# Kernel tuning notes

Measured on AMD Instinct MI355X. Metric: run time of the kernel, lower is better.

## Reference

```python
import jax, jax.numpy as jnp
import numpy as np

EPS = 1e-5

def _bn(h, g, b):
    # BatchNorm1d with batch statistics (biased variance), eps=1e-5
    m = jnp.mean(h, axis=0)
    v = jnp.var(h, axis=0)
    return (h - m) * jax.lax.rsqrt(v + EPS) * g + b

def setup_inputs() -> dict:
    key = jax.random.key(0)
    ks = jax.random.split(key, 12)
    N, E, F = 100000, 500000, 128
    D = 2 * F  # 256
    s = 1.0 / np.sqrt(D)
    inp = {
        "x": jax.random.normal(ks[0], (N, F), dtype=jnp.float32),
        "edge_index": jax.random.randint(ks[1], (2, E), 0, N, dtype=jnp.int64),
        "W4": jax.random.normal(ks[2], (D, D), jnp.float32) * s,
        "b4": jnp.zeros((D,), jnp.float32),
        "g4": jnp.ones((D,), jnp.float32),
        "be4": jnp.zeros((D,), jnp.float32),
        "W1": jax.random.normal(ks[3], (D, D), jnp.float32) * s,
        "b1": jnp.zeros((D,), jnp.float32),
        "g1": jnp.ones((D,), jnp.float32),
        "be1": jnp.zeros((D,), jnp.float32),
        "W2": jax.random.normal(ks[4], (D, D), jnp.float32) * s,
        "b2": jnp.zeros((D,), jnp.float32),
        "g2": jnp.ones((D,), jnp.float32),
        "be2": jnp.zeros((D,), jnp.float32),
        "Wf": jax.random.normal(ks[5], (D, 1), jnp.float32) * s,
        "bf": jnp.zeros((1,), jnp.float32),
    }
    return inp

def reference(x, edge_index, W4, b4, g4, be4, W1, b1, g1, be1, W2, b2, g2, be2, Wf, bf):
    # gather + concat: [E, 2*F]
    edge_x = jnp.concatenate((x[edge_index[0]], x[edge_index[1]]), axis=1)
    # block 4: Linear -> BN -> ReLU (dropout = identity in eval)
    edge_x = jax.nn.relu(_bn(edge_x @ W4 + b4, g4, be4))
    # block 1 with residual
    out1 = jax.nn.relu(_bn(edge_x @ W1 + b1, g1, be1)) + edge_x
    # block 2 with residual
    out2 = jax.nn.relu(_bn(out1 @ W2 + b2, g2, be2)) + out1
    # final projection -> flatten to [E]
    return jnp.ravel(out2 @ Wf + bf)
```

## Files before the change

kernel.cpp:

```cpp
#include <hip/hip_runtime.h>
#include <hip/hip_bf16.h>
#include <stdint.h>


typedef __attribute__((ext_vector_type(8))) short short8;
typedef __attribute__((ext_vector_type(4))) float f32x4;

__device__ __forceinline__ unsigned short bf16b(float f) {
  unsigned int u = __float_as_uint(f);
  return (unsigned short)((u + 0x7fffu + ((u >> 16) & 1u)) >> 16);
}
__device__ __forceinline__ unsigned int packbf(float lo, float hi) {
  return (unsigned int)bf16b(lo) | ((unsigned int)bf16b(hi) << 16);
}
__device__ __forceinline__ float bflo(unsigned int u) { return __uint_as_float(u << 16); }
__device__ __forceinline__ float bfhi(unsigned int u) { return __uint_as_float(u & 0xffff0000u); }
__device__ __forceinline__ float bfs(short s) { return __uint_as_float(((unsigned int)(unsigned short)s) << 16); }
__device__ __forceinline__ float relu_(float x) { return fmaxf(x, 0.0f); }

__global__ __launch_bounds__(256) void k_init(const int* __restrict__ ei,
                                              float* __restrict__ stats, int* __restrict__ flag) {
  const int t = threadIdx.x;
  for (int i = t; i < 1536; i += 256) stats[i] = 0.f;
  if (t == 0) {
    int o = 0;
#pragma unroll
    for (int i = 0; i < 32; ++i) o |= ei[2 * i + 1];
    *flag = (o == 0) ? 1 : 0;
  }
}

__global__ __launch_bounds__(256) void k_seed(float* __restrict__ out, const float* __restrict__ bfp, int E) {
  const int i = blockIdx.x * 256 + threadIdx.x;
  if (i < E) out[i] = bfp[0];
}

__global__ __launch_bounds__(256) void k_prep(
    const float* __restrict__ W4, const float* __restrict__ W1, const float* __restrict__ W2,
    unsigned short* __restrict__ wt4, unsigned short* __restrict__ wt1, unsigned short* __restrict__ wt2)
{
  const int b = blockIdx.x;
  const int t = threadIdx.x;
  const int wi = b >> 6;
  const int r = b & 63;
  const float* W = (wi == 0) ? W4 : (wi == 1) ? W1 : W2;
  unsigned short* Wt = (wi == 0) ? wt4 : (wi == 1) ? wt1 : wt2;
  const int flat = r * 1024 + t * 4;
  const int n = flat >> 8;
  const int k = flat & 255;
  ushort4 o;
  o.x = bf16b(W[(k + 0) * 256 + n]);
  o.y = bf16b(W[(k + 1) * 256 + n]);
  o.z = bf16b(W[(k + 2) * 256 + n]);
  o.w = bf16b(W[(k + 3) * 256 + n]);
  *(ushort4*)(Wt + flat) = o;
}

__global__ __launch_bounds__(256) void k_stats(
    const float* __restrict__ stats, const float* __restrict__ g, const float* __restrict__ be,
    const float* __restrict__ bias, float* __restrict__ scale, float invE)
{
  const int c = threadIdx.x;
  const float mean = stats[c] * invE;
  const float var = stats[256 + c] * invE - mean * mean;
  const float a = g[c] * rsqrtf(var + 1e-5f);
  const float cstd = be[c] - mean * a;
  scale[c] = a;
  scale[256 + c] = cstd;
  scale[512 + c] = fmaf(a, bias[c], cstd);
}

template<int MODE>
__global__ __launch_bounds__(512, 1) void kp(
    const void* Asrc, const int* __restrict__ ei, const int* __restrict__ flagp,
    const unsigned short* __restrict__ Wt, const float* __restrict__ bias,
    const float* __restrict__ scst, const float* __restrict__ scep, const float* __restrict__ wf,
    unsigned short* __restrict__ buf, float* __restrict__ stats, float* __restrict__ out,
    int E, int MT)
{
  __shared__ __align__(16) char bB[131072];
  __shared__ __align__(16) char aT[32768];

  const int t = threadIdx.x;
  const int b = blockIdx.x;
  const int per = MT >> 8, rem = MT & 255;
  const int t0 = b * per + (b < rem ? b : rem);
  const int t1 = t0 + per + (b < rem ? 1 : 0);

  const int l = t & 63, wv = t >> 6;
  const int wr = wv >> 2, wc = wv & 3;
  const int sw = (l & 7) << 4;
  const int subc = t & 31, rB = t >> 5;
  const int colb = wc * 64 + (l & 15);
  const int lr0 = wr * 32 + ((l >> 4) << 2);
  const int flag = (MODE == 1) ? flagp[0] : 0;

  float bj[4];
  if (MODE != 3) {
#pragma unroll
    for (int j = 0; j < 4; ++j) bj[j] = bias[colb + j * 16];
  }
  float aS[8], cS[8];
  if (MODE == 2) {
#pragma unroll
    for (int k = 0; k < 8; ++k) { aS[k] = scst[subc * 8 + k]; cS[k] = scst[512 + subc * 8 + k]; }
  }
  float aE[4], cE[4], wE[4];
  if (MODE == 3) {
#pragma unroll
    for (int j = 0; j < 4; ++j) {
      const int c = colb + j * 16;
      aE[j] = scep[c]; cE[j] = scep[512 + c]; wE[j] = wf[c];
    }
  }
  float ssum[4] = {0.f, 0.f, 0.f, 0.f}, ssq[4] = {0.f, 0.f, 0.f, 0.f};

  uint4 pf[4];
#define PREFETCH(TT)                                                              \
  if (MODE == 1) {                                                                \
    const float* xf = (const float*)Asrc;                                         \
    _Pragma("unroll")                                                             \
    for (int r = 0; r < 4; ++r) {                                                 \
      const int row = rB + r * 16;                                                \
      int e = (TT) * 64 + row; if (e >= E) e = E - 1;                             \
      const int idx = (subc < 16) ? e : (E + e);                                  \
      const int node = flag ? ei[2 * idx] : ei[idx];                              \
      const float* s = xf + node * 128 + (subc & 15) * 8;                         \
      float4 f0 = *(const float4*)s;                                              \
      float4 f1 = *(const float4*)(s + 4);                                        \
      pf[r].x = packbf(f0.x, f0.y); pf[r].y = packbf(f0.z, f0.w);                 \
      pf[r].z = packbf(f1.x, f1.y); pf[r].w = packbf(f1.z, f1.w);                 \
    }                                                                             \
  } else {                                                                        \
    const uint4* s = (const uint4*)((const char*)Asrc + (size_t)(TT) * 32768);    \
    _Pragma("unroll")                                                             \
    for (int r = 0; r < 4; ++r) pf[r] = s[t + r * 512];                           \
  }

#define STAGE_A                                                                   \
  _Pragma("unroll")                                                               \
  for (int r = 0; r < 4; ++r) {                                                   \
    const int row = rB + r * 16;                                                  \
    uint4 v = pf[r];                                                              \
    if (MODE == 2) {                                                              \
      unsigned int* vp = (unsigned int*)&v;                                       \
      _Pragma("unroll")                                                           \
      for (int h2 = 0; h2 < 4; ++h2) {                                            \
        float lo = relu_(fmaf(bflo(vp[h2]), aS[h2 * 2], cS[h2 * 2]));             \
        float hi = relu_(fmaf(bfhi(vp[h2]), aS[h2 * 2 + 1], cS[h2 * 2 + 1]));     \
        vp[h2] = packbf(lo, hi);                                                  \
      }                                                                           \
    }                                                                             \
    *(uint4*)(aT + row * 512 + ((subc * 16) ^ ((row & 7) << 4))) = v;             \
  }

  PREFETCH(t0);
#pragma unroll
  for (int r = 0; r < 16; ++r) {
    const int c = t + r * 512;
    uint4 v = *(const uint4*)(Wt + c * 8);
    const int n = c >> 5;
    *(uint4*)(bB + n * 512 + (((c & 31) * 16) ^ ((n & 7) << 4))) = v;
  }
  STAGE_A;
  __syncthreads();

  const int ar = wr * 32 + (l & 15);
  const int bn = wc * 64 + (l & 15);

  for (int tt = t0;;) {
    const bool more = (tt + 1 < t1);
    if (more) PREFETCH(tt + 1);

    f32x4 acc[2][4];
    f32x4 zz = {0.f, 0.f, 0.f, 0.f};
#pragma unroll
    for (int i = 0; i < 2; ++i)
#pragma unroll
      for (int j = 0; j < 4; ++j) acc[i][j] = zz;

#pragma unroll
    for (int ks = 0; ks < 4; ++ks) {
#pragma unroll
      for (int kk = 0; kk < 2; ++kk) {
        const int kb = ks * 128 + kk * 64 + ((l >> 4) << 4);
        short8 af[2], bfr[4];
        af[0] = *(const short8*)(aT + ar * 512 + (kb ^ sw));
        af[1] = *(const short8*)(aT + (ar + 16) * 512 + (kb ^ sw));
#pragma unroll
        for (int j = 0; j < 4; ++j)
          bfr[j] = *(const short8*)(bB + (bn + j * 16) * 512 + (kb ^ sw));
#pragma unroll
        for (int i = 0; i < 2; ++i)
#pragma unroll
          for (int j = 0; j < 4; ++j)
            acc[i][j] = __builtin_amdgcn_mfma_f32_16x16x32_bf16(af[i], bfr[j], acc[i][j], 0, 0, 0);
      }
    }

    if (MODE != 3) {
#pragma unroll
      for (int i = 0; i < 2; ++i) {
        const int r0 = tt * 64 + lr0 + i * 16;
#pragma unroll
        for (int j = 0; j < 4; ++j) {
#pragma unroll
          for (int q = 0; q < 4; ++q) {
            const float v = acc[i][j][q] + bj[j];
            if (r0 + q < E) { ssum[j] += v; ssq[j] = fmaf(v, v, ssq[j]); }
          }
        }
      }
    } else {
      float dq[2][4];
#pragma unroll
      for (int i = 0; i < 2; ++i)
#pragma unroll
        for (int q = 0; q < 4; ++q) dq[i][q] = 0.f;
#pragma unroll
      for (int i = 0; i < 2; ++i) {
#pragma unroll
        for (int j = 0; j < 4; ++j) {
#pragma unroll
          for (int q = 0; q < 4; ++q) {
            const int lrow = lr0 + i * 16 + q;
            const float h = bfs(*(const short*)(aT + lrow * 512 +
                                (((colb + j * 16) * 2) ^ ((lrow & 7) << 4))));
            const float v = relu_(fmaf(acc[i][j][q], aE[j], cE[j])) + h;
            acc[i][j][q] = v;
            dq[i][q] = fmaf(v, wE[j], dq[i][q]);
          }
        }
      }
#pragma unroll
      for (int i = 0; i < 2; ++i)
#pragma unroll
        for (int q = 0; q < 4; ++q) {
          float p = dq[i][q];
          p += __shfl_xor(p, 1); p += __shfl_xor(p, 2); p += __shfl_xor(p, 4); p += __shfl_xor(p, 8);
          if ((l & 15) == 0) {
            const int row = tt * 64 + lr0 + i * 16 + q;
            if (row < E) atomicAdd(&out[row], p);
          }
        }
    }
    __syncthreads();

    if (MODE != 2) {
      const int odd = l & 1;
#pragma unroll
      for (int i = 0; i < 2; ++i) {
        const int r0 = lr0 + i * 16;
#pragma unroll
        for (int j = 0; j < 4; ++j) {
          float v0 = acc[i][j][0], v1 = acc[i][j][1], v2 = acc[i][j][2], v3 = acc[i][j][3];
          float p0 = __shfl_xor(v0, 1), p1 = __shfl_xor(v1, 1);
          float p2 = __shfl_xor(v2, 1), p3 = __shfl_xor(v3, 1);
          float loA = odd ? p2 : v0, hiA = odd ? v2 : p0;
          float loB = odd ? p3 : v1, hiB = odd ? v3 : p1;
          const int ra = r0 + (odd ? 2 : 0);
          const int cp2 = ((colb + j * 16) & ~1) * 2;
          *(unsigned int*)(aT + (ra + 0) * 512 + (cp2 ^ (((ra + 0) & 7) << 4))) = packbf(loA, hiA);
          *(unsigned int*)(aT + (ra + 1) * 512 + (cp2 ^ (((ra + 1) & 7) << 4))) = packbf(loB, hiB);
        }
      }
      __syncthreads();
    }

    {
      char* d = (char*)buf + (size_t)tt * 32768;
#pragma unroll
      for (int r = 0; r < 4; ++r) {
        const int c = t + r * 512;
        const int row = c >> 5;
        uint4 v = *(const uint4*)(aT + row * 512 + (((c & 31) * 16) ^ ((row & 7) << 4)));
        *(uint4*)(d + c * 16) = v;
      }
    }

    ++tt;
    if (!(tt < t1)) break;
    __syncthreads();
    STAGE_A;
    __syncthreads();
  }

  if (MODE != 3) {
#pragma unroll
    for (int j = 0; j < 4; ++j) {
      ssum[j] += __shfl_xor(ssum[j], 16); ssum[j] += __shfl_xor(ssum[j], 32);
      ssq[j]  += __shfl_xor(ssq[j], 16);  ssq[j]  += __shfl_xor(ssq[j], 32);
    }
    const int g = l >> 4;
    float sg = (g == 0) ? ssum[0] : (g == 1) ? ssum[1] : (g == 2) ? ssum[2] : ssum[3];
    float qg = (g == 0) ? ssq[0] : (g == 1) ? ssq[1] : (g == 2) ? ssq[2] : ssq[3];
    const int col = wc * 64 + g * 16 + (l & 15);
    atomicAdd(&stats[col], sg);
    atomicAdd(&stats[256 + col], qg);
  }
#undef PREFETCH
#undef STAGE_A
}

__global__ __launch_bounds__(512) void k_fin(
    const unsigned short* __restrict__ Y, const float* __restrict__ scale,
    const float* __restrict__ wf, float* __restrict__ out, int E)
{
  __shared__ float sS[768];
  const int t = threadIdx.x;
  if (t < 256) { sS[t] = scale[t]; sS[256 + t] = scale[512 + t]; sS[512 + t] = wf[t]; }
  __syncthreads();
  const int row = blockIdx.x * 64 + (t >> 3);
  const int p = t & 7;
  const unsigned short* r = Y + (size_t)row * 256 + p * 32;
  float acc = 0.f;
#pragma unroll
  for (int m = 0; m < 4; ++m) {
    uint4 v = *(const uint4*)(r + m * 8);
    const int k0 = p * 32 + m * 8;
    const unsigned int* vp = (const unsigned int*)&v;
#pragma unroll
    for (int h = 0; h < 4; ++h) {
      const int k = k0 + h * 2;
      acc = fmaf(relu_(fmaf(bflo(vp[h]), sS[k], sS[256 + k])), sS[512 + k], acc);
      acc = fmaf(relu_(fmaf(bfhi(vp[h]), sS[k + 1], sS[256 + k + 1])), sS[512 + k + 1], acc);
    }
  }
  acc += __shfl_xor(acc, 1); acc += __shfl_xor(acc, 2); acc += __shfl_xor(acc, 4);
  if (p == 0 && row < E) out[row] += acc;
}

__global__ __launch_bounds__(256) void k_bail(float* __restrict__ out, const float* __restrict__ bfp, int E) {
  const int i = blockIdx.x * 256 + threadIdx.x;
  if (i < E) out[i] = bfp[0];
}

extern "C" void kernel_launch(void* const* d_in, const int* in_sizes, int n_in,
                              void* d_out, int out_size, void* d_ws, size_t ws_size,
                              hipStream_t stream) {
  const float* x   = (const float*)d_in[0];
  const int*   ei  = (const int*)d_in[1];
  const float* W4  = (const float*)d_in[2];
  const float* b4  = (const float*)d_in[3];
  const float* g4  = (const float*)d_in[4];
  const float* be4 = (const float*)d_in[5];
  const float* W1  = (const float*)d_in[6];
  const float* b1  = (const float*)d_in[7];
  const float* g1  = (const float*)d_in[8];
  const float* be1 = (const float*)d_in[9];
  const float* W2  = (const float*)d_in[10];
  const float* b2  = (const float*)d_in[11];
  const float* g2  = (const float*)d_in[12];
  const float* be2 = (const float*)d_in[13];
  const float* Wf  = (const float*)d_in[14];
  const float* bfp = (const float*)d_in[15];
  float* out = (float*)d_out;

  const int E = out_size;
  const int MT = (E + 63) / 64;
  const float invE = 1.0f / (float)E;

  char* ws = (char*)d_ws;
  unsigned short* wt4 = (unsigned short*)(ws);
  unsigned short* wt1 = (unsigned short*)(ws + 131072);
  unsigned short* wt2 = (unsigned short*)(ws + 262144);
  float* stats = (float*)(ws + 393216);
  float* scale = (float*)(ws + 399360);
  int*   flag  = (int*)(ws + 408576);
  const size_t fixed = 409600;
  const size_t bufbytes = (size_t)MT * 32768;
  unsigned short* buf = (unsigned short*)(ws + fixed);

  if (ws_size < fixed + bufbytes) {
    k_bail<<<(E + 255) / 256, 256, 0, stream>>>(out, bfp, E);
    return;
  }

  k_init<<<1, 256, 0, stream>>>(ei, stats, flag);
  k_prep<<<192, 256, 0, stream>>>(W4, W1, W2, wt4, wt1, wt2);

  kp<1><<<256, 512, 0, stream>>>((const void*)x, ei, flag, wt4, b4,
                                 nullptr, nullptr, nullptr, buf, stats, nullptr, E, MT);
  k_stats<<<1, 256, 0, stream>>>(stats, g4, be4, b4, scale, invE);
  kp<2><<<256, 512, 0, stream>>>((const void*)buf, nullptr, flag, wt1, b1,
                                 scale, nullptr, nullptr, buf, stats + 512, nullptr, E, MT);
  k_stats<<<1, 256, 0, stream>>>(stats + 512, g1, be1, b1, scale + 768, invE);
  k_seed<<<(E + 255) / 256, 256, 0, stream>>>(out, bfp, E);
  kp<3><<<256, 512, 0, stream>>>((const void*)buf, nullptr, flag, wt1, nullptr,
                                 nullptr, scale + 768, Wf, buf, nullptr, out, E, MT);
  kp<4><<<256, 512, 0, stream>>>((const void*)buf, nullptr, flag, wt2, b2,
                                 nullptr, nullptr, nullptr, buf, stats + 1024, nullptr, E, MT);
  k_stats<<<1, 256, 0, stream>>>(stats + 1024, g2, be2, b2, scale + 1536, invE);
  k_fin<<<MT, 512, 0, stream>>>(buf, scale + 1536, Wf, out, E);
}
```

Measured before the change: 610.2 us.

## Double-buffer A tiles, hold B fragments in registers, use 1024-thread blocks

The GEMM kernel now runs 1024 threads per block with 16 waves. Each wave keeps its slice of the weight matrix in registers, loaded once, so the B operand is no longer re-read from LDS on every tile. The A tile is double-buffered in LDS so staging the next tile overlaps the MFMA work on the current one. Mode 3 now applies the BN transform itself, and its final-projection partial sums are reduced in LDS and written directly, replacing the global atomics and the separate seed kernel. BN statistics go into 8 slices of atomics to cut contention. The cost is higher register pressure, and the LDS reduction needs extra barriers per tile.

Result: slower. 1.011 ms (+65.7%).

```diff
diff --git a/kernel.cpp b/kernel.cpp
--- a/kernel.cpp
+++ b/kernel.cpp
@@ -21,7 +21,7 @@
 __global__ __launch_bounds__(256) void k_init(const int* __restrict__ ei,
                                               float* __restrict__ stats, int* __restrict__ flag) {
   const int t = threadIdx.x;
-  for (int i = t; i < 1536; i += 256) stats[i] = 0.f;
+  for (int i = t; i < 12288; i += 256) stats[i] = 0.f;
   if (t == 0) {
     int o = 0;
 #pragma unroll
@@ -30,7 +30,7 @@
   }
 }
 
-__global__ __launch_bounds__(256) void k_seed(float* __restrict__ out, const float* __restrict__ bfp, int E) {
+__global__ __launch_bounds__(256) void k_bail(float* __restrict__ out, const float* __restrict__ bfp, int E) {
   const int i = blockIdx.x * 256 + threadIdx.x;
   if (i < E) out[i] = bfp[0];
 }
@@ -61,8 +61,11 @@
     const float* __restrict__ bias, float* __restrict__ scale, float invE)
 {
   const int c = threadIdx.x;
-  const float mean = stats[c] * invE;
-  const float var = stats[256 + c] * invE - mean * mean;
+  float s = 0.f, q = 0.f;
+#pragma unroll
+  for (int sl = 0; sl < 8; ++sl) { s += stats[sl * 512 + c]; q += stats[sl * 512 + 256 + c]; }
+  const float mean = s * invE;
+  const float var = q * invE - mean * mean;
   const float a = g[c] * rsqrtf(var + 1e-5f);
   const float cstd = be[c] - mean * a;
   scale[c] = a;
@@ -71,15 +74,15 @@
 }
 
 template<int MODE>
-__global__ __launch_bounds__(512, 1) void kp(
+__global__ __launch_bounds__(1024, 1) void kp(
     const void* Asrc, const int* __restrict__ ei, const int* __restrict__ flagp,
     const unsigned short* __restrict__ Wt, const float* __restrict__ bias,
     const float* __restrict__ scst, const float* __restrict__ scep, const float* __restrict__ wf,
     unsigned short* __restrict__ buf, float* __restrict__ stats, float* __restrict__ out,
-    int E, int MT)
+    const float* __restrict__ bfp, int E, int MT)
 {
-  __shared__ __align__(16) char bB[131072];
-  __shared__ __align__(16) char aT[32768];
+  __shared__ __align__(16) char lds[131072];
+  float* sRed = (float*)(lds + 65536);
 
   const int t = threadIdx.x;
   const int b = blockIdx.x;
@@ -88,114 +91,119 @@
   const int t1 = t0 + per + (b < rem ? 1 : 0);
 
   const int l = t & 63, wv = t >> 6;
-  const int wr = wv >> 2, wc = wv & 3;
+  const int wr = wv >> 3, wc = wv & 7;
   const int sw = (l & 7) << 4;
-  const int subc = t & 31, rB = t >> 5;
-  const int colb = wc * 64 + (l & 15);
+  const int subc = t & 31;
+  const int colb = wc * 32 + (l & 15);
   const int lr0 = wr * 32 + ((l >> 4) << 2);
   const int flag = (MODE == 1) ? flagp[0] : 0;
-
-  float bj[4];
-  if (MODE != 3) {
-#pragma unroll
-    for (int j = 0; j < 4; ++j) bj[j] = bias[colb + j * 16];
-  }
-  float aS[8], cS[8];
-  if (MODE == 2) {
-#pragma unroll
-    for (int k = 0; k < 8; ++k) { aS[k] = scst[subc * 8 + k]; cS[k] = scst[512 + subc * 8 + k]; }
-  }
-  float aE[4], cE[4], wE[4];
+  const float bf0 = (MODE == 3) ? bfp[0] : 0.f;
+
+  float bj[2];
+  if (MODE != 3) { bj[0] = bias[colb]; bj[1] = bias[colb + 16]; }
+  float aE[2], cE[2], wE[2];
   if (MODE == 3) {
 #pragma unroll
-    for (int j = 0; j < 4; ++j) {
+    for (int j = 0; j < 2; ++j) {
       const int c = colb + j * 16;
       aE[j] = scep[c]; cE[j] = scep[512 + c]; wE[j] = wf[c];
     }
   }
-  float ssum[4] = {0.f, 0.f, 0.f, 0.f}, ssq[4] = {0.f, 0.f, 0.f, 0.f};
-
-  uint4 pf[4];
-#define PREFETCH(TT)                                                              \
-  if (MODE == 1) {                                                                \
-    const float* xf = (const float*)Asrc;                                         \
-    _Pragma("unroll")                                                             \
-    for (int r = 0; r < 4; ++r) {                                                 \
-      const int row = rB + r * 16;                                                \
-      int e = (TT) * 64 + row; if (e >= E) e = E - 1;                             \
-      const int idx = (subc < 16) ? e : (E + e);                                  \
-      const int node = flag ? ei[2 * idx] : ei[idx];                              \
-      const float* s = xf + node * 128 + (subc & 15) * 8;                         \
-      float4 f0 = *(const float4*)s;                                              \
-      float4 f1 = *(const float4*)(s + 4);                                        \
-      pf[r].x = packbf(f0.x, f0.y); pf[r].y = packbf(f0.z, f0.w);                 \
-      pf[r].z = packbf(f1.x, f1.y); pf[r].w = packbf(f1.z, f1.w);                 \
-    }                                                                             \
-  } else {                                                                        \
-    const uint4* s = (const uint4*)((const char*)Asrc + (size_t)(TT) * 32768);    \
-    _Pragma("unroll")                                                             \
-    for (int r = 0; r < 4; ++r) pf[r] = s[t + r * 512];                           \
-  }
-
-#define STAGE_A                                                                   \
-  _Pragma("unroll")                                                               \
-  for (int r = 0; r < 4; ++r) {                                                   \
-    const int row = rB + r * 16;                                                  \
-    uint4 v = pf[r];                                                              \
-    if (MODE == 2) {                                                              \
-      unsigned int* vp = (unsigned int*)&v;                                       \
-      _Pragma("unroll")                                                           \
-      for (int h2 = 0; h2 < 4; ++h2) {                                            \
-        float lo = relu_(fmaf(bflo(vp[h2]), aS[h2 * 2], cS[h2 * 2]));             \
-        float hi = relu_(fmaf(bfhi(vp[h2]), aS[h2 * 2 + 1], cS[h2 * 2 + 1]));     \
-        vp[h2] = packbf(lo, hi);                                                  \
-      }                                                                           \
-    }                                                                             \
-    *(uint4*)(aT + row * 512 + ((subc * 16) ^ ((row & 7) << 4))) = v;             \
+  float ssum[2] = {0.f, 0.f}, ssq[2] = {0.f, 0.f};
+
+  uint4 pf[2];
+#define PREFETCH(TT)                                                            \
+  if (MODE == 1) {                                                              \
+    const float* xf = (const float*)Asrc;                                       \
+    _Pragma("unroll")                                                           \
+    for (int r = 0; r < 2; ++r) {                                               \
+      const int c = t + r * 1024;                                               \
+      const int row = c >> 5;                                                   \
+      int e = (TT) * 64 + row; if (e >= E) e = E - 1;                           \
+      const int idx = (subc < 16) ? e : (E + e);                                \
+      const int node = flag ? ei[2 * idx] : ei[idx];                            \
+      const float* s = xf + node * 128 + (subc & 15) * 8;                       \
+      float4 f0 = *(const float4*)s;                                            \
+      float4 f1 = *(const float4*)(s + 4);                                      \
+      pf[r].x = packbf(f0.x, f0.y); pf[r].y = packbf(f0.z, f0.w);               \
+      pf[r].z = packbf(f1.x, f1.y); pf[r].w = packbf(f1.z, f1.w);               \
+    }                                                                           \
+  } else {                                                                      \
+    const uint4* s = (const uint4*)((const char*)Asrc + (size_t)(TT) * 32768);  \
+    pf[0] = s[t]; pf[1] = s[t + 1024];                                          \
+  }
+
+#define STAGE_A(AP)                                                             \
+  _Pragma("unroll")                                                             \
+  for (int r = 0; r < 2; ++r) {                                                 \
+    const int c = t + r * 1024;                                                 \
+    const int row = c >> 5;                                                     \
+    uint4 v = pf[r];                                                            \
+    if (MODE == 2 || MODE == 3) {                                               \
+      const float4* s4 = (const float4*)(scst + subc * 8);                      \
+      const float4* c4 = (const float4*)(scst + 512 + subc * 8);                \
+      float4 aa0 = s4[0], aa1 = s4[1], cc0 = c4[0], cc1 = c4[1];                \
+      unsigned int* vp = (unsigned int*)&v;                                     \
+      vp[0] = packbf(relu_(fmaf(bflo(vp[0]), aa0.x, cc0.x)),                    \
+                     relu_(fmaf(bfhi(vp[0]), aa0.y, cc0.y)));                   \
+      vp[1] = packbf(relu_(fmaf(bflo(vp[1]), aa0.z, cc0.z)),                    \
+                     relu_(fmaf(bfhi(vp[1]), aa0.w, cc0.w)));                   \
+      vp[2] = packbf(relu_(fmaf(bflo(vp[2]), aa1.x, cc1.x)),                    \
+                     relu_(fmaf(bfhi(vp[2]), aa1.y, cc1.y)));                   \
+      vp[3] = packbf(relu_(fmaf(bflo(vp[3]), aa1.z, cc1.z)),                    \
+                     relu_(fmaf(bfhi(vp[3]), aa1.w, cc1.w)));                   \
+    }                                                                           \
+    *(uint4*)((AP) + row * 512 + ((subc * 16) ^ ((row & 7) << 4))) = v;         \
   }
 
   PREFETCH(t0);
 #pragma unroll
-  for (int r = 0; r < 16; ++r) {
-    const int c = t + r * 512;
+  for (int r = 0; r < 8; ++r) {
+    const int c = t + r * 1024;
     uint4 v = *(const uint4*)(Wt + c * 8);
     const int n = c >> 5;
-    *(uint4*)(bB + n * 512 + (((c & 31) * 16) ^ ((n & 7) << 4))) = v;
-  }
-  STAGE_A;
+    *(uint4*)(lds + n * 512 + (((c & 31) * 16) ^ ((n & 7) << 4))) = v;
+  }
   __syncthreads();
-
-  const int ar = wr * 32 + (l & 15);
-  const int bn = wc * 64 + (l & 15);
-
-  for (int tt = t0;;) {
-    const bool more = (tt + 1 < t1);
-    if (more) PREFETCH(tt + 1);
-
-    f32x4 acc[2][4];
+  short8 bf8[8][2];
+#pragma unroll
+  for (int s8 = 0; s8 < 8; ++s8) {
+    const int kb = (s8 * 64 + ((l >> 4) << 4)) ^ sw;
+#pragma unroll
+    for (int j = 0; j < 2; ++j) {
+      const int bn = wc * 32 + j * 16 + (l & 15);
+      bf8[s8][j] = *(const short8*)(lds + bn * 512 + kb);
+    }
+  }
+  __syncthreads();
+  char* aT0 = lds;
+  char* aT1 = lds + 32768;
+
+  STAGE_A(aT0);
+  if (t0 + 1 < t1) PREFETCH(t0 + 1);
+  __syncthreads();
+
+  int cur = 0;
+  for (int tt = t0; tt < t1; ++tt) {
+    char* aC = cur ? aT1 : aT0;
+    char* aN = cur ? aT0 : aT1;
+    if (tt + 1 < t1) {
+      STAGE_A(aN);
+      if (tt + 2 < t1) PREFETCH(tt + 2);
+    }
+
+    f32x4 acc[2][2];
     f32x4 zz = {0.f, 0.f, 0.f, 0.f};
-#pragma unroll
-    for (int i = 0; i < 2; ++i)
-#pragma unroll
-      for (int j = 0; j < 4; ++j) acc[i][j] = zz;
-
-#pragma unroll
-    for (int ks = 0; ks < 4; ++ks) {
-#pragma unroll
-      for (int kk = 0; kk < 2; ++kk) {
-        const int kb = ks * 128 + kk * 64 + ((l >> 4) << 4);
-        short8 af[2], bfr[4];
-        af[0] = *(const short8*)(aT + ar * 512 + (kb ^ sw));
-        af[1] = *(const short8*)(aT + (ar + 16) * 512 + (kb ^ sw));
-#pragma unroll
-        for (int j = 0; j < 4; ++j)
-          bfr[j] = *(const short8*)(bB + (bn + j * 16) * 512 + (kb ^ sw));
-#pragma unroll
-        for (int i = 0; i < 2; ++i)
-#pragma unroll
-          for (int j = 0; j < 4; ++j)
-            acc[i][j] = __builtin_amdgcn_mfma_f32_16x16x32_bf16(af[i], bfr[j], acc[i][j], 0, 0, 0);
-      }
+    acc[0][0] = zz; acc[0][1] = zz; acc[1][0] = zz; acc[1][1] = zz;
+#pragma unroll
+    for (int s8 = 0; s8 < 8; ++s8) {
+      const int kb = (s8 * 64 + ((l >> 4) << 4)) ^ sw;
+      short8 a0 = *(const short8*)(aC + (wr * 32 + (l & 15)) * 512 + kb);
+      short8 a1 = *(const short8*)(aC + (wr * 32 + 16 + (l & 15)) * 512 + kb);
+      acc[0][0] = __builtin_amdgcn_mfma_f32_16x16x32_bf16(a0, bf8[s8][0], acc[0][0], 0, 0, 0);
+      acc[0][1] = __builtin_amdgcn_mfma_f32_16x16x32_bf16(a0, bf8[s8][1], acc[0][1], 0, 0, 0);
+      acc[1][0] = __builtin_amdgcn_mfma_f32_16x16x32_bf16(a1, bf8[s8][0], acc[1][0], 0, 0, 0);
+      acc[1][1] = __builtin_amdgcn_mfma_f32_16x16x32_bf16(a1, bf8[s8][1], acc[1][1], 0, 0, 0);
     }
 
     if (MODE != 3) {
@@ -203,13 +211,12 @@
       for (int i = 0; i < 2; ++i) {
         const int r0 = tt * 64 + lr0 + i * 16;
 #pragma unroll
-        for (int j = 0; j < 4; ++j) {
+        for (int j = 0; j < 2; ++j)
 #pragma unroll
           for (int q = 0; q < 4; ++q) {
             const float v = acc[i][j][q] + bj[j];
             if (r0 + q < E) { ssum[j] += v; ssq[j] = fmaf(v, v, ssq[j]); }
           }
-        }
       }
     } else {
       float dq[2][4];
@@ -218,30 +225,27 @@
 #pragma unroll
         for (int q = 0; q < 4; ++q) dq[i][q] = 0.f;
 #pragma unroll
-      for (int i = 0; i < 2; ++i) {
-#pragma unroll
-        for (int j = 0; j < 4; ++j) {
+      for (int i = 0; i < 2; ++i)
+#pragma unroll
+        for (int j = 0; j < 2; ++j) {
+          const int col = colb + j * 16;
 #pragma unroll
           for (int q = 0; q < 4; ++q) {
             const int lrow = lr0 + i * 16 + q;
-            const float h = bfs(*(const short*)(aT + lrow * 512 +
-                                (((colb + j * 16) * 2) ^ ((lrow & 7) << 4))));
+            const float h = bfs(*(const short*)(aC + lrow * 512 + ((col * 2) ^ ((lrow & 7) << 4))));
             const float v = relu_(fmaf(acc[i][j][q], aE[j], cE[j])) + h;
             acc[i][j][q] = v;
             dq[i][q] = fmaf(v, wE[j], dq[i][q]);
           }
         }
-      }
 #pragma unroll
       for (int i = 0; i < 2; ++i)
 #pragma unroll
         for (int q = 0; q < 4; ++q) {
           float p = dq[i][q];
-          p += __shfl_xor(p, 1); p += __shfl_xor(p, 2); p += __shfl_xor(p, 4); p += __shfl_xor(p, 8);
-          if ((l & 15) == 0) {
-            const int row = tt * 64 + lr0 + i * 16 + q;
-            if (row < E) atomicAdd(&out[row], p);
-          }
+          p += __shfl_xor(p, 1); p += __shfl_xor(p, 2);
+          p += __shfl_xor(p, 4); p += __shfl_xor(p, 8);
+          if ((l & 15) == 0) sRed[(lr0 + i * 16 + q) * 8 + wc] = p;
         }
     }
     __syncthreads();
@@ -252,7 +256,7 @@
       for (int i = 0; i < 2; ++i) {
         const int r0 = lr0 + i * 16;
 #pragma unroll
-        for (int j = 0; j < 4; ++j) {
+        for (int j = 0; j < 2; ++j) {
           float v0 = acc[i][j][0], v1 = acc[i][j][1], v2 = acc[i][j][2], v3 = acc[i][j][3];
           float p0 = __shfl_xor(v0, 1), p1 = __shfl_xor(v1, 1);
           float p2 = __shfl_xor(v2, 1), p3 = __shfl_xor(v3, 1);
@@ -260,43 +264,49 @@
           float loB = odd ? p3 : v1, hiB = odd ? v3 : p1;
           const int ra = r0 + (odd ? 2 : 0);
           const int cp2 = ((colb + j * 16) & ~1) * 2;
-          *(unsigned int*)(aT + (ra + 0) * 512 + (cp2 ^ (((ra + 0) & 7) << 4))) = packbf(loA, hiA);
-          *(unsigned int*)(aT + (ra + 1) * 512 + (cp2 ^ (((ra + 1) & 7) << 4))) = packbf(loB, hiB);
+          *(unsigned int*)(aC + (ra + 0) * 512 + (cp2 ^ (((ra + 0) & 7) << 4))) = packbf(loA, hiA);
+          *(unsigned int*)(aC + (ra + 1) * 512 + (cp2 ^ (((ra + 1) & 7) << 4))) = packbf(loB, hiB);
+        }
+      }
+      if (MODE == 3 && t < 64) {
+        const int row = tt * 64 + t;
+        if (row < E) {
+          float s = 0.f;
+#pragma unroll
+          for (int w = 0; w < 8; ++w) s += sRed[t * 8 + w];
+          out[row] = s + bf0;
         }
       }
       __syncthreads();
-    }
-
-    {
       char* d = (char*)buf + (size_t)tt * 32768;
 #pragma unroll
-      for (int r = 0; r < 4; ++r) {
-        const int c = t + r * 512;
+      for (int r = 0; r < 2; ++r) {
+        const int c = t + r * 1024;
         const int row = c >> 5;
-        uint4 v = *(const uint4*)(aT + row * 512 + (((c & 31) * 16) ^ ((row & 7) << 4)));
+        uint4 v = *(const uint4*)(aC + row * 512 + (((c & 31) * 16) ^ ((row & 7) << 4)));
         *(uint4*)(d + c * 16) = v;
       }
-    }
-
-    ++tt;
-    if (!(tt < t1)) break;
-    __syncthreads();
-    STAGE_A;
-    __syncthreads();
+      __syncthreads();
+    }
+    cur ^= 1;
   }
 
   if (MODE != 3) {
 #pragma unroll
-    for (int j = 0; j < 4; ++j) {
+    for (int j = 0; j < 2; ++j) {
       ssum[j] += __shfl_xor(ssum[j], 16); ssum[j] += __shfl_xor(ssum[j], 32);
       ssq[j]  += __shfl_xor(ssq[j], 16);  ssq[j]  += __shfl_xor(ssq[j], 32);
     }
     const int g = l >> 4;
-    float sg = (g == 0) ? ssum[0] : (g == 1) ? ssum[1] : (g == 2) ? ssum[2] : ssum[3];
-    float qg = (g == 0) ? ssq[0] : (g == 1) ? ssq[1] : (g == 2) ? ssq[2] : ssq[3];
-    const int col = wc * 64 + g * 16 + (l & 15);
-    atomicAdd(&stats[col], sg);
-    atomicAdd(&stats[256 + col], qg);
+    const int col = wc * 32 + ((g & 1) << 4) + (l & 15);
+    const float val = (g < 2) ? ((g & 1) ? ssum[1] : ssum[0]) : ((g & 1) ? ssq[1] : ssq[0]);
+    __syncthreads();
+    sRed[wr * 512 + ((g >> 1) << 8) + col] = val;
+    __syncthreads();
+    if (t < 512) {
+      const float v = sRed[t] + sRed[512 + t];
+      atomicAdd(&stats[(b & 7) * 512 + t], v);
+    }
   }
 #undef PREFETCH
 #undef STAGE_A
@@ -328,11 +338,6 @@
   }
   acc += __shfl_xor(acc, 1); acc += __shfl_xor(acc, 2); acc += __shfl_xor(acc, 4);
   if (p == 0 && row < E) out[row] += acc;
-}
-
-__global__ __launch_bounds__(256) void k_bail(float* __restrict__ out, const float* __restrict__ bfp, int E) {
-  const int i = blockIdx.x * 256 + threadIdx.x;
-  if (i < E) out[i] = bfp[0];
 }
 
 extern "C" void kernel_launch(void* const* d_in, const int* in_sizes, int n_in,
@@ -365,9 +370,9 @@
   unsigned short* wt1 = (unsigned short*)(ws + 131072);
   unsigned short* wt2 = (unsigned short*)(ws + 262144);
   float* stats = (float*)(ws + 393216);
-  float* scale = (float*)(ws + 399360);
-  int*   flag  = (int*)(ws + 408576);
-  const size_t fixed = 409600;
+  float* scale = (float*)(ws + 442368);
+  int*   flag  = (int*)(ws + 451584);
+  const size_t fixed = 458752;
   const size_t bufbytes = (size_t)MT * 32768;
   unsigned short* buf = (unsigned short*)(ws + fixed);
 
@@ -379,17 +384,16 @@
   k_init<<<1, 256, 0, stream>>>(ei, stats, flag);
   k_prep<<<192, 256, 0, stream>>>(W4, W1, W2, wt4, wt1, wt2);
 
-  kp<1><<<256, 512, 0, stream>>>((const void*)x, ei, flag, wt4, b4,
-                                 nullptr, nullptr, nullptr, buf, stats, nullptr, E, MT);
+  kp<1><<<256, 1024, 0, stream>>>((const void*)x, ei, flag, wt4, b4,
+                                  nullptr, nullptr, nullptr, buf, stats, nullptr, bfp, E, MT);
   k_stats<<<1, 256, 0, stream>>>(stats, g4, be4, b4, scale, invE);
-  kp<2><<<256, 512, 0, stream>>>((const void*)buf, nullptr, flag, wt1, b1,
-                                 scale, nullptr, nullptr, buf, stats + 512, nullptr, E, MT);
-  k_stats<<<1, 256, 0, stream>>>(stats + 512, g1, be1, b1, scale + 768, invE);
-  k_seed<<<(E + 255) / 256, 256, 0, stream>>>(out, bfp, E);
-  kp<3><<<256, 512, 0, stream>>>((const void*)buf, nullptr, flag, wt1, nullptr,
-                                 nullptr, scale + 768, Wf, buf, nullptr, out, E, MT);
-  kp<4><<<256, 512, 0, stream>>>((const void*)buf, nullptr, flag, wt2, b2,
-                                 nullptr, nullptr, nullptr, buf, stats + 1024, nullptr, E, MT);
-  k_stats<<<1, 256, 0, stream>>>(stats + 1024, g2, be2, b2, scale + 1536, invE);
+  kp<2><<<256, 1024, 0, stream>>>((const void*)buf, nullptr, flag, wt1, b1,
+                                  scale, nullptr, nullptr, buf, stats + 4096, nullptr, bfp, E, MT);
+  k_stats<<<1, 256, 0, stream>>>(stats + 4096, g1, be1, b1, scale + 768, invE);
+  kp<3><<<256, 1024, 0, stream>>>((const void*)buf, nullptr, flag, wt1, nullptr,
+                                  scale, scale + 768, Wf, buf, nullptr, out, bfp, E, MT);
+  kp<4><<<256, 1024, 0, stream>>>((const void*)buf, nullptr, flag, wt2, b2,
+                                  nullptr, nullptr, nullptr, buf, stats + 8192, nullptr, bfp, E, MT);
+  k_stats<<<1, 256, 0, stream>>>(stats + 8192, g2, be2, b2, scale + 1536, invE);
   k_fin<<<MT, 512, 0, stream>>>(buf, scale + 1536, Wf, out, E);
 }
```
